# Kernel optimization log

Measured on AMD Instinct MI355X. Metric: run time of the kernel, lower is better.

Reference implementation:

```python
import jax, jax.numpy as jnp
import numpy as np

B, T, D, H, O = 256, 512, 128, 128, 64


def setup_inputs() -> dict:
    key = jax.random.key(0)
    ks = jax.random.split(key, 10)
    s = 1.0 / np.sqrt(H)
    u = lambda k, shape: jax.random.uniform(k, shape, jnp.float32, -s, s)
    return {
        "x": jax.random.normal(ks[0], (B, T, D), jnp.float32),
        "W_ih": u(ks[1], (4 * H, D)),   # torch gate order: i, f, g, o
        "W_hh": u(ks[2], (4 * H, H)),
        "b_ih": u(ks[3], (4 * H,)),
        "b_hh": u(ks[4], (4 * H,)),
        "W1": u(ks[5], (H, H)),
        "b1": u(ks[6], (H,)),
        "W2": u(ks[7], (O, H)),
        "b2": u(ks[8], (O,)),
    }


def lstm_scan(x, W_ih, W_hh, b_ih, b_hh):
    b, t, _ = x.shape
    h4 = W_hh.shape[0] // 4
    # precompute input contribution for all timesteps (one big GEMM)
    xg = jnp.einsum('btd,gd->btg', x, W_ih) + b_ih + b_hh  # (B,T,4H)
    xg = jnp.swapaxes(xg, 0, 1)  # (T,B,4H) for scan over time

    def step(carry, xg_t):
        h, c = carry
        g = xg_t + h @ W_hh.T  # (B,4H)
        i, f, gg, o = jnp.split(g, 4, axis=-1)
        i = jax.nn.sigmoid(i)
        f = jax.nn.sigmoid(f)
        gg = jnp.tanh(gg)
        o = jax.nn.sigmoid(o)
        c = f * c + i * gg
        h = o * jnp.tanh(c)
        return (h, c), h

    h0 = jnp.zeros((b, h4), x.dtype)
    c0 = jnp.zeros((b, h4), x.dtype)
    _, hs = jax.lax.scan(step, (h0, c0), xg)  # hs: (T,B,H)
    return jnp.swapaxes(hs, 0, 1)  # (B,T,H), matching torch batch_first


def reference(x, W_ih, W_hh, b_ih, b_hh, W1, b1, W2, b2):
    b, t, _ = x.shape
    h = lstm_scan(x, W_ih, W_hh, b_ih, b_hh)          # (B,T,H)
    hflat = h.reshape(-1, h.shape[-1])                 # (B*T,H), b-major (as torch)
    hflat = hflat @ W1.T + b1
    y = hflat @ W2.T + b2                              # (B*T,O)
    # faithful to original: reshape flattened b-major rows as (T,B,O), take [-1]
    y = y.reshape(t, b, -1)
    return y[-1]                                       # (B,O)
```

## Files before the change

kernel.cpp:

```cpp
#include <hip/hip_runtime.h>
#include <math.h>

#define BB 256
#define TT 512
#define DD 128
#define HH 128
#define GG 512
#define OO 64
#define NCH (TT / 4)

typedef _Float16 half8 __attribute__((ext_vector_type(8)));
typedef float    f32x4 __attribute__((ext_vector_type(4)));

__device__ __forceinline__ float sigmoid_fast(float x) {
    return 1.0f / (1.0f + __expf(-x));
}
__device__ __forceinline__ float tanh_fast(float x) {
    float ax = fabsf(x);
    float e = __expf(2.0f * ax);
    float t = 1.0f - 2.0f / (e + 1.0f);
    return copysignf(t, x);
}

__global__ __launch_bounds__(256) void wpack_kernel(
    const float* __restrict__ Wf, _Float16* __restrict__ Wp)
{
    const int g = blockIdx.x * 256 + threadIdx.x;
    const int fid = g >> 6, l = g & 63;
    const int w = fid >> 5, rem = fid & 31, nt = rem >> 2, kt = rem & 3;
    const int quad = l >> 4, col = l & 15;
    const int row = (nt >> 1) * 128 + (nt & 1) * 16 + w * 32 + col;
    const int off = kt * 32 + quad * 8;
    const float* s = Wf + row * HH + off;
    _Float16* d = Wp + (size_t)g * 8;
#pragma unroll
    for (int i = 0; i < 8; i++) d[i] = (_Float16)s[i];
}

__global__ __launch_bounds__(512) void xg_kernel(
    const float* __restrict__ x,
    const float* __restrict__ W_ih,
    const float* __restrict__ b_ih,
    const float* __restrict__ b_hh,
    float* __restrict__ xg)
{
    const int t = blockIdx.x;
    const int g = threadIdx.x;

    __shared__ __align__(16) float xs[DD];
    if (g < DD) xs[g] = x[(255 * TT + t) * DD + g];
    __syncthreads();

    const float4* __restrict__ wrow = (const float4*)(W_ih + g * DD);
    const float4* __restrict__ xv   = (const float4*)xs;

    float a0 = 0.f, a1 = 0.f, a2 = 0.f, a3 = 0.f;
#pragma unroll
    for (int i = 0; i < DD / 4; i += 4) {
        float4 w0 = wrow[i + 0], w1 = wrow[i + 1], w2 = wrow[i + 2], w3 = wrow[i + 3];
        float4 h0 = xv[i + 0],  h1 = xv[i + 1],  h2 = xv[i + 2],  h3 = xv[i + 3];
        a0 += w0.x * h0.x + w0.y * h0.y + w0.z * h0.z + w0.w * h0.w;
        a1 += w1.x * h1.x + w1.y * h1.y + w1.z * h1.z + w1.w * h1.w;
        a2 += w2.x * h2.x + w2.y * h2.y + w2.z * h2.z + w2.w * h2.w;
        a3 += w3.x * h3.x + w3.y * h3.y + w3.z * h3.z + w3.w * h3.w;
    }
    const float val = (a0 + a1) + (a2 + a3) + b_ih[g] + b_hh[g];
    xg[t * GG + (g & 127) * 4 + (g >> 7)] = val;
}

__global__
__attribute__((amdgpu_flat_work_group_size(256, 256), amdgpu_waves_per_eu(1, 1)))
void scan_kernel(
    const _Float16* __restrict__ Wp,
    const float* __restrict__ xgp,
    float* __restrict__ hs)
{
    const int tid  = threadIdx.x;
    const int lane = tid & 63;
    const int w    = tid >> 6;
    const int col  = lane & 15;
    const int quad = lane >> 4;
    const int wbase = w * 32;
    const bool sel  = (lane >= 32);
    const int jsel  = wbase + (sel ? 16 : 0) + col;
    const int aoff  = quad * 8;

    __shared__ __align__(16) _Float16 h_lds[2][HH];
    __shared__ __align__(16) float xgc[2][4][HH][4];
    __shared__ __align__(16) float hs_l[BB * HH];

#define BLOADP(nt, kt) \
    half8 B##nt##_##kt = *(const half8*)(Wp + (((w * 32 + (nt) * 4 + (kt)) * 64 + lane) * 8));
#define FOR_KT(X, nt) X(nt, 0) X(nt, 1) X(nt, 2) X(nt, 3)
#define FOR_NT(X) FOR_KT(X, 0) FOR_KT(X, 1) FOR_KT(X, 2) FOR_KT(X, 3) \
                  FOR_KT(X, 4) FOR_KT(X, 5) FOR_KT(X, 6) FOR_KT(X, 7)
    FOR_NT(BLOADP)

    if (tid < HH) h_lds[0][tid] = (_Float16)0.f;

    {
        const f32x4* src = (const f32x4*)xgp;
        f32x4 a = src[2 * tid], b = src[2 * tid + 1];
        f32x4* dst = (f32x4*)&xgc[0][0][0][0];
        dst[2 * tid] = a; dst[2 * tid + 1] = b;
    }
    float c = 0.f;
    int p = 0;
    __syncthreads();

    f32x4 pf0, pf1;

    for (int ch = 0; ch < NCH; ch++) {
        const int buf = ch & 1;
        if (ch + 1 < NCH) {
            const f32x4* src = (const f32x4*)(xgp + (ch + 1) * 4 * GG);
            pf0 = src[2 * tid];
            pf1 = src[2 * tid + 1];
        }
#pragma unroll
        for (int k = 0; k < 4; k++) {
            const int t = ch * 4 + k;

            const _Float16* hl = h_lds[p];
            half8 A0 = *(const half8*)(hl + 0 * 32 + aoff);
            half8 A1 = *(const half8*)(hl + 1 * 32 + aoff);
            half8 A2 = *(const half8*)(hl + 2 * 32 + aoff);
            half8 A3 = *(const half8*)(hl + 3 * 32 + aoff);

            f32x4 xgv = *(const f32x4*)&xgc[buf][k][jsel][0];

            f32x4 C0 = {0.f,0.f,0.f,0.f}, C1 = {0.f,0.f,0.f,0.f};
            f32x4 C2 = {0.f,0.f,0.f,0.f}, C3 = {0.f,0.f,0.f,0.f};
            f32x4 C4 = {0.f,0.f,0.f,0.f}, C5 = {0.f,0.f,0.f,0.f};
            f32x4 C6 = {0.f,0.f,0.f,0.f}, C7 = {0.f,0.f,0.f,0.f};
#define MF(nt, kt) \
            C##nt = __builtin_amdgcn_mfma_f32_16x16x32_f16(A##kt, B##nt##_##kt, C##nt, 0, 0, 0);
#define MF_ALLNT(kt) MF(0, kt) MF(1, kt) MF(2, kt) MF(3, kt) \
                     MF(4, kt) MF(5, kt) MF(6, kt) MF(7, kt)
            MF_ALLNT(0) MF_ALLNT(1) MF_ALLNT(2) MF_ALLNT(3)

            float pi = (sel ? C1[0] : C0[0]) + xgv.x;
            float pf = (sel ? C3[0] : C2[0]) + xgv.y;
            float pg = (sel ? C5[0] : C4[0]) + xgv.z;
            float po = (sel ? C7[0] : C6[0]) + xgv.w;

            float iv = sigmoid_fast(pi);
            float fv = sigmoid_fast(pf);
            float gv = tanh_fast(pg);
            float ov = sigmoid_fast(po);

            c = fv * c + iv * gv;
            float hval = ov * tanh_fast(c);

            if (quad == 0 || quad == 3) {
                h_lds[1 - p][jsel] = (_Float16)hval;
                if (t >= TT - BB) hs_l[(t - (TT - BB)) * HH + jsel] = hval;
            }

            if (k == 3 && ch + 1 < NCH) {
                f32x4* dst = (f32x4*)&xgc[1 - buf][0][0][0];
                dst[2 * tid] = pf0;
                dst[2 * tid + 1] = pf1;
            }

            p ^= 1;
            __syncthreads();
        }
    }

    const f32x4* s = (const f32x4*)hs_l;
    f32x4* d = (f32x4*)hs;
#pragma unroll 4
    for (int i = tid; i < BB * HH / 4; i += 256) d[i] = s[i];
}

__global__ __launch_bounds__(128) void mlp_kernel(
    const float* __restrict__ hs,
    const float* __restrict__ W1,
    const float* __restrict__ b1,
    const float* __restrict__ W2,
    const float* __restrict__ b2,
    float* __restrict__ out)
{
    const int r = blockIdx.x;
    const int j = threadIdx.x;

    __shared__ __align__(16) float hsh[HH];
    __shared__ __align__(16) float z[HH];

    hsh[j] = hs[r * HH + j];
    __syncthreads();

    {
        const float4* __restrict__ wrow = (const float4*)(W1 + j * HH);
        const float4* __restrict__ hv   = (const float4*)hsh;
        float acc = b1[j];
#pragma unroll
        for (int i = 0; i < 32; i++) {
            float4 ww = wrow[i], h = hv[i];
            acc += ww.x * h.x + ww.y * h.y + ww.z * h.z + ww.w * h.w;
        }
        z[j] = acc;
    }
    __syncthreads();

    if (j < OO) {
        const float4* __restrict__ wrow = (const float4*)(W2 + j * HH);
        const float4* __restrict__ zv   = (const float4*)z;
        float acc = b2[j];
#pragma unroll
        for (int i = 0; i < 32; i++) {
            float4 ww = wrow[i], zz = zv[i];
            acc += ww.x * zz.x + ww.y * zz.y + ww.z * zz.z + ww.w * zz.w;
        }
        out[r * OO + j] = acc;
    }
}

extern "C" void kernel_launch(void* const* d_in, const int* in_sizes, int n_in,
                              void* d_out, int out_size, void* d_ws, size_t ws_size,
                              hipStream_t stream) {
    const float* x    = (const float*)d_in[0];
    const float* W_ih = (const float*)d_in[1];
    const float* W_hh = (const float*)d_in[2];
    const float* b_ih = (const float*)d_in[3];
    const float* b_hh = (const float*)d_in[4];
    const float* W1   = (const float*)d_in[5];
    const float* b1   = (const float*)d_in[6];
    const float* W2   = (const float*)d_in[7];
    const float* b2   = (const float*)d_in[8];
    float* out = (float*)d_out;

    float*    xg = (float*)d_ws;
    float*    hs = xg + TT * GG;
    _Float16* Wp = (_Float16*)(hs + BB * HH);

    wpack_kernel<<<32, 256, 0, stream>>>(W_hh, Wp);
    xg_kernel<<<TT, 512, 0, stream>>>(x, W_ih, b_ih, b_hh, xg);
    scan_kernel<<<1, 256, 0, stream>>>(Wp, xg, hs);
    mlp_kernel<<<BB, 128, 0, stream>>>(hs, W1, b1, W2, b2, out);
}
```

Baseline: 388.8 us.

## Split LSTM scan across eight waves and fold weight packing into xg kernel

The single-block recurrent scan now uses 512 threads (8 waves), each owning 16 hidden units, so each wave issues 16 MFMAs per step instead of 32. The xg bias term is seeded into the MFMA accumulators, which drops the post-MFMA adds and lane selects. The W_hh fp16 packing moves into extra blocks of the xg kernel, removing one launch. The cost is a per-step barrier across 8 waves instead of 4, and only a quarter of lanes doing useful gate math.

Measured after the change: 429.2 us. +10.4%, slower.

```diff
diff --git a/kernel.cpp b/kernel.cpp
--- a/kernel.cpp
+++ b/kernel.cpp
@@ -22,28 +22,29 @@
     return copysignf(t, x);
 }
 
-__global__ __launch_bounds__(256) void wpack_kernel(
-    const float* __restrict__ Wf, _Float16* __restrict__ Wp)
-{
-    const int g = blockIdx.x * 256 + threadIdx.x;
-    const int fid = g >> 6, l = g & 63;
-    const int w = fid >> 5, rem = fid & 31, nt = rem >> 2, kt = rem & 3;
-    const int quad = l >> 4, col = l & 15;
-    const int row = (nt >> 1) * 128 + (nt & 1) * 16 + w * 32 + col;
-    const int off = kt * 32 + quad * 8;
-    const float* s = Wf + row * HH + off;
-    _Float16* d = Wp + (size_t)g * 8;
-#pragma unroll
-    for (int i = 0; i < 8; i++) d[i] = (_Float16)s[i];
-}
-
-__global__ __launch_bounds__(512) void xg_kernel(
+__global__ __launch_bounds__(512) void xgpack_kernel(
     const float* __restrict__ x,
     const float* __restrict__ W_ih,
     const float* __restrict__ b_ih,
     const float* __restrict__ b_hh,
-    float* __restrict__ xg)
+    const float* __restrict__ W_hh,
+    float* __restrict__ xg,
+    _Float16* __restrict__ Wp)
 {
+    if (blockIdx.x >= TT) {
+        const int g = (blockIdx.x - TT) * 512 + threadIdx.x;
+        const int fid = g >> 6, l = g & 63;
+        const int w = fid >> 4, gt = (fid >> 2) & 3, kt = fid & 3;
+        const int quad = l >> 4, col = l & 15;
+        const int row = gt * 128 + w * 16 + col;
+        const int off = kt * 32 + quad * 8;
+        const float* s = W_hh + row * HH + off;
+        _Float16* d = Wp + (size_t)g * 8;
+#pragma unroll
+        for (int i = 0; i < 8; i++) d[i] = (_Float16)s[i];
+        return;
+    }
+
     const int t = blockIdx.x;
     const int g = threadIdx.x;
 
@@ -69,7 +70,7 @@
 }
 
 __global__
-__attribute__((amdgpu_flat_work_group_size(256, 256), amdgpu_waves_per_eu(1, 1)))
+__attribute__((amdgpu_flat_work_group_size(512, 512), amdgpu_waves_per_eu(2, 2)))
 void scan_kernel(
     const _Float16* __restrict__ Wp,
     const float* __restrict__ xgp,
@@ -80,42 +81,37 @@
     const int w    = tid >> 6;
     const int col  = lane & 15;
     const int quad = lane >> 4;
-    const int wbase = w * 32;
-    const bool sel  = (lane >= 32);
-    const int jsel  = wbase + (sel ? 16 : 0) + col;
-    const int aoff  = quad * 8;
+    const int jsel = w * 16 + col;
+    const int aoff = quad * 8;
 
     __shared__ __align__(16) _Float16 h_lds[2][HH];
     __shared__ __align__(16) float xgc[2][4][HH][4];
     __shared__ __align__(16) float hs_l[BB * HH];
 
-#define BLOADP(nt, kt) \
-    half8 B##nt##_##kt = *(const half8*)(Wp + (((w * 32 + (nt) * 4 + (kt)) * 64 + lane) * 8));
-#define FOR_KT(X, nt) X(nt, 0) X(nt, 1) X(nt, 2) X(nt, 3)
-#define FOR_NT(X) FOR_KT(X, 0) FOR_KT(X, 1) FOR_KT(X, 2) FOR_KT(X, 3) \
-                  FOR_KT(X, 4) FOR_KT(X, 5) FOR_KT(X, 6) FOR_KT(X, 7)
-    FOR_NT(BLOADP)
+#define BLOADP(gt, kt) \
+    half8 B##gt##_##kt = *(const half8*)(Wp + (((w * 16 + (gt) * 4 + (kt)) * 64 + lane) * 8));
+    BLOADP(0,0) BLOADP(0,1) BLOADP(0,2) BLOADP(0,3)
+    BLOADP(1,0) BLOADP(1,1) BLOADP(1,2) BLOADP(1,3)
+    BLOADP(2,0) BLOADP(2,1) BLOADP(2,2) BLOADP(2,3)
+    BLOADP(3,0) BLOADP(3,1) BLOADP(3,2) BLOADP(3,3)
 
     if (tid < HH) h_lds[0][tid] = (_Float16)0.f;
 
     {
         const f32x4* src = (const f32x4*)xgp;
-        f32x4 a = src[2 * tid], b = src[2 * tid + 1];
-        f32x4* dst = (f32x4*)&xgc[0][0][0][0];
-        dst[2 * tid] = a; dst[2 * tid + 1] = b;
+        f32x4 a = src[tid];
+        ((f32x4*)&xgc[0][0][0][0])[tid] = a;
     }
     float c = 0.f;
     int p = 0;
     __syncthreads();
 
-    f32x4 pf0, pf1;
+    f32x4 pf;
 
     for (int ch = 0; ch < NCH; ch++) {
         const int buf = ch & 1;
         if (ch + 1 < NCH) {
-            const f32x4* src = (const f32x4*)(xgp + (ch + 1) * 4 * GG);
-            pf0 = src[2 * tid];
-            pf1 = src[2 * tid + 1];
+            pf = ((const f32x4*)(xgp + (ch + 1) * 4 * GG))[tid];
         }
 #pragma unroll
         for (int k = 0; k < 4; k++) {
@@ -128,39 +124,34 @@
             half8 A3 = *(const half8*)(hl + 3 * 32 + aoff);
 
             f32x4 xgv = *(const f32x4*)&xgc[buf][k][jsel][0];
-
-            f32x4 C0 = {0.f,0.f,0.f,0.f}, C1 = {0.f,0.f,0.f,0.f};
-            f32x4 C2 = {0.f,0.f,0.f,0.f}, C3 = {0.f,0.f,0.f,0.f};
-            f32x4 C4 = {0.f,0.f,0.f,0.f}, C5 = {0.f,0.f,0.f,0.f};
-            f32x4 C6 = {0.f,0.f,0.f,0.f}, C7 = {0.f,0.f,0.f,0.f};
-#define MF(nt, kt) \
-            C##nt = __builtin_amdgcn_mfma_f32_16x16x32_f16(A##kt, B##nt##_##kt, C##nt, 0, 0, 0);
-#define MF_ALLNT(kt) MF(0, kt) MF(1, kt) MF(2, kt) MF(3, kt) \
-                     MF(4, kt) MF(5, kt) MF(6, kt) MF(7, kt)
-            MF_ALLNT(0) MF_ALLNT(1) MF_ALLNT(2) MF_ALLNT(3)
-
-            float pi = (sel ? C1[0] : C0[0]) + xgv.x;
-            float pf = (sel ? C3[0] : C2[0]) + xgv.y;
-            float pg = (sel ? C5[0] : C4[0]) + xgv.z;
-            float po = (sel ? C7[0] : C6[0]) + xgv.w;
-
-            float iv = sigmoid_fast(pi);
-            float fv = sigmoid_fast(pf);
-            float gv = tanh_fast(pg);
-            float ov = sigmoid_fast(po);
+            f32x4 C0 = {xgv.x, 0.f, 0.f, 0.f};
+            f32x4 C1 = {xgv.y, 0.f, 0.f, 0.f};
+            f32x4 C2 = {xgv.z, 0.f, 0.f, 0.f};
+            f32x4 C3 = {xgv.w, 0.f, 0.f, 0.f};
+
+#define MF(gt, kt) \
+            C##gt = __builtin_amdgcn_mfma_f32_16x16x32_f16(A##kt, B##gt##_##kt, C##gt, 0, 0, 0);
+            MF(0,0) MF(1,0) MF(2,0) MF(3,0)
+            MF(0,1) MF(1,1) MF(2,1) MF(3,1)
+            MF(0,2) MF(1,2) MF(2,2) MF(3,2)
+            MF(0,3) MF(1,3) MF(2,3) MF(3,3)
+#undef MF
+
+            float iv = sigmoid_fast(C0[0]);
+            float fv = sigmoid_fast(C1[0]);
+            float gv = tanh_fast(C2[0]);
+            float ov = sigmoid_fast(C3[0]);
 
             c = fv * c + iv * gv;
             float hval = ov * tanh_fast(c);
 
-            if (quad == 0 || quad == 3) {
+            if (quad == 0) {
                 h_lds[1 - p][jsel] = (_Float16)hval;
                 if (t >= TT - BB) hs_l[(t - (TT - BB)) * HH + jsel] = hval;
             }
 
             if (k == 3 && ch + 1 < NCH) {
-                f32x4* dst = (f32x4*)&xgc[1 - buf][0][0][0];
-                dst[2 * tid] = pf0;
-                dst[2 * tid + 1] = pf1;
+                ((f32x4*)&xgc[1 - buf][0][0][0])[tid] = pf;
             }
 
             p ^= 1;
@@ -171,7 +162,7 @@
     const f32x4* s = (const f32x4*)hs_l;
     f32x4* d = (f32x4*)hs;
 #pragma unroll 4
-    for (int i = tid; i < BB * HH / 4; i += 256) d[i] = s[i];
+    for (int i = tid; i < BB * HH / 4; i += 512) d[i] = s[i];
 }
 
 __global__ __launch_bounds__(128) void mlp_kernel(
@@ -235,8 +226,7 @@
     float*    hs = xg + TT * GG;
     _Float16* Wp = (_Float16*)(hs + BB * HH);
 
-    wpack_kernel<<<32, 256, 0, stream>>>(W_hh, Wp);
-    xg_kernel<<<TT, 512, 0, stream>>>(x, W_ih, b_ih, b_hh, xg);
-    scan_kernel<<<1, 256, 0, stream>>>(Wp, xg, hs);
+    xgpack_kernel<<<TT + 16, 512, 0, stream>>>(x, W_ih, b_ih, b_hh, W_hh, xg, Wp);
+    scan_kernel<<<1, 512, 0, stream>>>(Wp, xg, hs);
     mlp_kernel<<<BB, 128, 0, stream>>>(hs, W1, b1, W2, b2, out);
 }
```
